# Optimization experiments

Measured on AMD Instinct MI355X. Metric: run time of the kernel, lower is better.

## Reference

```python
import jax, jax.numpy as jnp
import numpy as np

L, N, C = 8192, 8, 3
DIM, DIM_OUT, K, RATIO = 64, 128, 16, 0.25
L2 = int(L * RATIO)  # 2048; note L % L2 == 0 (needed for the fmod quirk)
EPS = 1e-5


def layer_norm(x, g, b):
    m = jnp.mean(x, axis=-1, keepdims=True)
    v = jnp.mean(jnp.square(x - m), axis=-1, keepdims=True)  # biased var, as torch LayerNorm
    return (x - m) * jax.lax.rsqrt(v + EPS) * g + b


def mlp(x, w1, g1, b1, w2, g2, b2):
    h = x @ w1.T
    h = layer_norm(h, g1, b1)
    h = h @ w2.T
    h = layer_norm(h, g2, b2)
    return jax.nn.relu(h)


def setup_inputs() -> dict:
    key = jax.random.key(0)
    ks = jax.random.split(key, 5)
    coords = jax.random.normal(ks[0], (L, N, C), jnp.float32)
    features = jax.random.normal(ks[1], (L, N, DIM), jnp.float32)
    s1 = 1.0 / np.sqrt(DIM)
    s2 = 1.0 / np.sqrt(DIM_OUT)
    w1 = jax.random.uniform(ks[2], (DIM_OUT, DIM), jnp.float32, -s1, s1)
    w2 = jax.random.uniform(ks[3], (DIM_OUT, DIM_OUT), jnp.float32, -s2, s2)
    g1 = jnp.ones((DIM_OUT,), jnp.float32)
    b1 = jnp.zeros((DIM_OUT,), jnp.float32)
    g2 = jnp.ones((DIM_OUT,), jnp.float32)
    b2 = jnp.zeros((DIM_OUT,), jnp.float32)
    # RandomDecimate: random permutation of point indices, keep first L2 (same across batch)
    keep_idx = jax.random.permutation(ks[4], L)[:L2].astype(jnp.int32)
    return dict(coords=coords, features=features, w1=w1, g1=g1, b1=b1,
                w2=w2, g2=g2, b2=b2, keep_idx=keep_idx)


def reference(coords, features, w1, g1, b1, w2, g2, b2, keep_idx):
    # MLP on all points: [L, N, DIM_OUT]
    feats = mlp(features, w1, g1, b1, w2, g2, b2)
    # decimation: keep_coords [L2, N, C]
    keep_coords = coords[keep_idx]
    # per-batch KNN of kept points against all points
    c = coords.transpose(1, 0, 2)        # [N, L, C]
    kc = keep_coords.transpose(1, 0, 2)  # [N, L2, C]
    d2 = (jnp.sum(kc * kc, -1)[:, :, None]
          + jnp.sum(c * c, -1)[:, None, :]
          - 2.0 * jnp.einsum('nic,njc->nij', kc, c))  # [N, L2, L]
    _, nn_idx = jax.lax.top_k(-d2, K)    # [N, L2, K] indices into [0, L)
    # faithful to clusters.fmod_(L2) on flattened idx n*L+l (L % L2 == 0 => l % L2)
    nn_idx = nn_idx % L2
    # fused gather + amax pooling over K neighbors
    fT = feats.transpose(1, 0, 2)  # [N, L, DIM_OUT]
    gathered = jax.vmap(lambda f, idx: f[idx])(fT, nn_idx)  # [N, L2, K, DIM_OUT]
    pool_features = jnp.max(gathered, axis=2).transpose(1, 0, 2)  # [L2, N, DIM_OUT]
    return keep_coords, pool_features
```

## Files before the change

### kernel.cpp

```cpp
#include <hip/hip_runtime.h>
#include <stdint.h>

#define L_    8192
#define N_    8
#define L2_   2048
#define K_    16

typedef unsigned int uint;
typedef unsigned short ushort;
typedef unsigned long long u64;
typedef __attribute__((ext_vector_type(8))) short bh8;
typedef __attribute__((ext_vector_type(4))) float f32x4;

__device__ __forceinline__ ushort f2b(float f){
  uint u = __float_as_uint(f);
  return (ushort)((u + 0x7FFFu + ((u >> 16) & 1u)) >> 16);
}
__device__ __forceinline__ uint ford(float f){
  uint u = __float_as_uint(f);
  return u ^ ((uint)((int)u >> 31) | 0x80000000u);
}
__device__ __forceinline__ float unford(uint u){
  uint v = (u & 0x80000000u) ? (u ^ 0x80000000u) : ~u;
  return __uint_as_float(v);
}

__device__ __forceinline__ void ld8(float* t, const float* p){
  float4 a = *(const float4*)p; float4 b = *(const float4*)(p + 4);
  t[0]=a.x; t[1]=a.y; t[2]=a.z; t[3]=a.w; t[4]=b.x; t[5]=b.y; t[6]=b.z; t[7]=b.w;
}
__device__ __forceinline__ bh8 pack8(const float* v){
  bh8 r;
  #pragma unroll
  for (int j = 0; j < 8; ++j) r[j] = (short)f2b(v[j]);
  return r;
}

__global__ __launch_bounds__(256) void prep_pack_k(const float* __restrict__ coords,
                                                   const int* __restrict__ keep,
                                                   const float* __restrict__ w1,
                                                   const float* __restrict__ w2,
                                                   float4* __restrict__ cF,
                                                   float* __restrict__ out0,
                                                   ushort* __restrict__ pw1,
                                                   ushort* __restrict__ pw2){
  int blk = blockIdx.x;
  int tid = threadIdx.x;
  if (blk < 96){
    int e = blk * 256 + tid;
    if (e < 8192) pw1[e] = f2b(w1[e]);
    else          pw2[e - 8192] = f2b(w2[e - 8192]);
  } else if (blk < 352){
    int e = (blk - 96) * 256 + tid;
    int l = e >> 3, n = e & 7;
    const float* cr = coords + (size_t)e * 3;
    float x = cr[0], y = cr[1], z = cr[2];
    float cc;
    {
      #pragma clang fp contract(off)
      cc = x*x + y*y + z*z;
    }
    cF[n * L_ + l] = make_float4(x, y, z, cc);
  } else {
    int t = (blk - 352) * 256 + tid;
    int i = t / 24; int rem = t - i * 24;
    out0[t] = coords[(size_t)keep[i] * 24 + rem];
  }
}

__global__ __launch_bounds__(256) void mlp_k(const float* __restrict__ feat,
                                             const ushort* __restrict__ pw1,
                                             const float* __restrict__ g1,
                                             const float* __restrict__ b1,
                                             const ushort* __restrict__ pw2,
                                             const float* __restrict__ g2,
                                             const float* __restrict__ b2,
                                             uint* __restrict__ fBw){
  __shared__ ushort hlds[64 * 136];
  int tid = threadIdx.x;
  int lane = tid & 63;
  int wv = __builtin_amdgcn_readfirstlane(tid >> 6);
  int quad = lane >> 4, c = lane & 15;
  int rowg = blockIdx.x * 64 + wv * 16;

  bh8 a1[2];
  {
    int rg = rowg + c; int l = rg & 2047, nb = rg >> 11;
    const float* xr = feat + (size_t)((l << 3) + nb) * 64 + quad * 8;
    float t[8];
    ld8(t, xr);      a1[0] = pack8(t);
    ld8(t, xr + 32); a1[1] = pack8(t);
  }

  f32x4 acc1[8];
  #pragma unroll
  for (int t = 0; t < 8; ++t) acc1[t] = (f32x4){0.f, 0.f, 0.f, 0.f};
  #pragma unroll
  for (int s = 0; s < 2; ++s){
    #pragma unroll
    for (int t = 0; t < 8; ++t){
      bh8 wb = *(const bh8*)(pw1 + (size_t)(t * 16 + c) * 64 + s * 32 + quad * 8);
      acc1[t] = __builtin_amdgcn_mfma_f32_16x16x32_bf16(a1[s], wb, acc1[t], 0, 0, 0);
    }
  }

  float mean1[4], rstd1[4];
  #pragma unroll
  for (int r = 0; r < 4; ++r){
    float s = 0.f;
    #pragma unroll
    for (int t = 0; t < 8; ++t) s += acc1[t][r];
    #pragma unroll
    for (int m = 1; m < 16; m <<= 1) s += __shfl_xor(s, m, 16);
    mean1[r] = s * 0.0078125f;
  }
  #pragma unroll
  for (int r = 0; r < 4; ++r){
    float s = 0.f;
    #pragma unroll
    for (int t = 0; t < 8; ++t){ float d = acc1[t][r] - mean1[r]; s += d * d; }
    #pragma unroll
    for (int m = 1; m < 16; m <<= 1) s += __shfl_xor(s, m, 16);
    rstd1[r] = rsqrtf(s * 0.0078125f + 1e-5f);
  }
  ushort* hl = hlds + wv * 16 * 136;
  #pragma unroll
  for (int t = 0; t < 8; ++t){
    float gv = g1[t * 16 + c], bv = b1[t * 16 + c];
    #pragma unroll
    for (int r = 0; r < 4; ++r){
      float v = (acc1[t][r] - mean1[r]) * rstd1[r] * gv + bv;
      hl[(quad * 4 + r) * 136 + t * 16 + c] = f2b(v);
    }
  }

  f32x4 acc2[8];
  #pragma unroll
  for (int t = 0; t < 8; ++t) acc2[t] = (f32x4){0.f, 0.f, 0.f, 0.f};
  #pragma unroll
  for (int s = 0; s < 4; ++s){
    bh8 af = *(const bh8*)(hl + c * 136 + s * 32 + quad * 8);
    #pragma unroll
    for (int t = 0; t < 8; ++t){
      bh8 wb = *(const bh8*)(pw2 + (size_t)(t * 16 + c) * 128 + s * 32 + quad * 8);
      acc2[t] = __builtin_amdgcn_mfma_f32_16x16x32_bf16(af, wb, acc2[t], 0, 0, 0);
    }
  }

  float mean2[4], rstd2[4];
  #pragma unroll
  for (int r = 0; r < 4; ++r){
    float s = 0.f;
    #pragma unroll
    for (int t = 0; t < 8; ++t) s += acc2[t][r];
    #pragma unroll
    for (int m = 1; m < 16; m <<= 1) s += __shfl_xor(s, m, 16);
    mean2[r] = s * 0.0078125f;
  }
  #pragma unroll
  for (int r = 0; r < 4; ++r){
    float s = 0.f;
    #pragma unroll
    for (int t = 0; t < 8; ++t){ float d = acc2[t][r] - mean2[r]; s += d * d; }
    #pragma unroll
    for (int m = 1; m < 16; m <<= 1) s += __shfl_xor(s, m, 16);
    rstd2[r] = rsqrtf(s * 0.0078125f + 1e-5f);
  }
  #pragma unroll
  for (int t = 0; t < 8; ++t){
    float gv = g2[t * 16 + c], bv = b2[t * 16 + c];
    #pragma unroll
    for (int r = 0; r < 4; ++r){
      float v = fmaxf((acc2[t][r] - mean2[r]) * rstd2[r] * gv + bv, 0.f);
      hl[(quad * 4 + r) * 136 + t * 16 + c] = f2b(v);
    }
  }

  {
    int row16 = lane >> 2, chunk = lane & 3;
    const uint* src = (const uint*)hlds + (wv * 16 + row16) * 68 + chunk * 16;
    uint* dst = fBw + (size_t)(rowg + row16) * 64 + chunk * 16;
    #pragma unroll
    for (int j = 0; j < 4; ++j)
      *(uint4*)(dst + j * 4) = *(const uint4*)(src + j * 4);
  }
}

__device__ __forceinline__ u64 shfl64(u64 v, int src){
  int lo = __shfl((int)(uint)v, src, 64);
  int hi = __shfl((int)(uint)(v >> 32), src, 64);
  return ((u64)(uint)hi << 32) | (uint)lo;
}

__device__ __forceinline__ u64 bsort64(u64 key, int lane){
  #pragma unroll
  for (int k = 2; k <= 64; k <<= 1){
    #pragma unroll
    for (int j = k >> 1; j > 0; j >>= 1){
      u64 o = shfl64(key, lane ^ j);
      bool lower = (lane & j) == 0;
      bool down  = (lane & k) == 0;
      bool takeMin = (lower == down);
      bool oLess = o < key;
      key = (oLess == takeMin) ? o : key;
    }
  }
  return key;
}
__device__ __forceinline__ u64 bmerge64(u64 key, int lane){
  #pragma unroll
  for (int j = 32; j > 0; j >>= 1){
    u64 o = shfl64(key, lane ^ j);
    bool lower = (lane & j) == 0;
    bool oLess = o < key;
    key = (oLess == lower) ? o : key;
  }
  return key;
}

__device__ __attribute__((noinline)) u64 drainx(u64* ldsq, int qcount, int lane){
  u64 a = (lane < qcount) ? ldsq[lane] : ~0ull;
  a = bsort64(a, lane);
  if (qcount > 64){
    u64 b = (64 + lane < qcount) ? ldsq[64 + lane] : ~0ull;
    b = bsort64(b, lane);
    u64 br = shfl64(b, 63 - lane);
    a = a < br ? a : br;
    a = bmerge64(a, lane);
  }
  if (lane < 16) ldsq[lane] = a;
  return a;
}

__device__ __forceinline__ void updq(u64* ql, int& qc, int& nx, float& thr,
                                     float qw, int lane){
  int q = qc;
  u64 k0 = (lane < q) ? ql[lane] : ~0ull;
  u64 k1 = (64 + lane < q) ? ql[64 + lane] : ~0ull;
  uint h0 = (uint)(k0 >> 32), h1 = (uint)(k1 >> 32);
  uint m = h0 < h1 ? h0 : h1;
  uint v = 0u;
  #pragma unroll
  for (int b = 31; b >= 16; --b){
    uint tv = v | (1u << b);
    if (__popcll(__ballot(m < tv)) < 16) v = tv;
  }
  uint vb = (v >= 0xFFFF0000u) ? 0xFFFFFFFFu : (v + 0x10000u);

  bool kp0 = (h0 <= vb);
  u64 bal0 = __ballot(kp0);
  int r0 = __builtin_amdgcn_mbcnt_lo((uint)bal0, 0);
  r0 = __builtin_amdgcn_mbcnt_hi((uint)(bal0 >> 32), r0);
  if (kp0) ql[r0] = k0;
  int c0 = __popcll(bal0);
  bool kp1 = (h1 <= vb);
  u64 bal1 = __ballot(kp1);
  int r1 = __builtin_amdgcn_mbcnt_lo((uint)bal1, 0);
  r1 = __builtin_amdgcn_mbcnt_hi((uint)(bal1 >> 32), r1);
  if (kp1) ql[c0 + r1] = k1;
  int out = c0 + __popcll(bal1);

  uint hb = vb;
  if (out > 64){
    u64 a = drainx(ql, out, lane);
    hb = (uint)(shfl64(a, 15) >> 32);
    out = 16;
  }
  qc = out;
  nx = out + 33;
  thr = unford(hb) + 1e-3f - qw;
}

__global__ __launch_bounds__(256) void knn_pool_k(const float4* __restrict__ cF,
                                                  const int* __restrict__ keep,
                                                  const uint* __restrict__ fB32,
                                                  float* __restrict__ out1){
  __shared__ u64 q8[4][2][128];
  int tid = threadIdx.x, lane = tid & 63;
  int wv = tid >> 6;
  int g0 = blockIdx.x * 8 + wv * 2;
  int n = g0 >> 11;
  int i0 = g0 & 2047, i1 = i0 + 1;
  u64* qlA = q8[wv][0];
  u64* qlB = q8[wv][1];
  float4 qa = cF[(n << 13) + keep[i0]];
  float4 qb = cF[(n << 13) + keep[i1]];
  const float4* base = cF + (n << 13);

  float q2ax = -2.f * qa.x, q2ay = -2.f * qa.y, q2az = -2.f * qa.z;
  float q2bx = -2.f * qb.x, q2by = -2.f * qb.y, q2bz = -2.f * qb.z;
  float tA = 3.4e38f, tB = 3.4e38f;
  int qcA = 0, qcB = 0, nxA = 49, nxB = 49;

  #define PROC2(cf, jidx) { \
    float sA = __builtin_fmaf(q2ax,(cf).x, __builtin_fmaf(q2ay,(cf).y, __builtin_fmaf(q2az,(cf).z,(cf).w))); \
    float sB = __builtin_fmaf(q2bx,(cf).x, __builtin_fmaf(q2by,(cf).y, __builtin_fmaf(q2bz,(cf).z,(cf).w))); \
    u64 balA = __ballot(sA <= tA); \
    u64 balB = __ballot(sB <= tB); \
    if (balA){ \
      if (sA <= tA){ \
        float d2; \
        { \
          _Pragma("clang fp contract(off)") \
          float dot = qa.x*(cf).x + qa.y*(cf).y + qa.z*(cf).z; \
          d2 = (qa.w + (cf).w) - 2.0f * dot; \
        } \
        int rel = __builtin_amdgcn_mbcnt_lo((uint)balA, 0); \
        rel = __builtin_amdgcn_mbcnt_hi((uint)(balA >> 32), rel); \
        qlA[qcA + rel] = ((u64)ford(d2) << 32) | (uint)(jidx); \
      } \
      qcA += __popcll(balA); \
      if (qcA >= nxA) updq(qlA, qcA, nxA, tA, qa.w, lane); \
    } \
    if (balB){ \
      if (sB <= tB){ \
        float d2; \
        { \
          _Pragma("clang fp contract(off)") \
          float dot = qb.x*(cf).x + qb.y*(cf).y + qb.z*(cf).z; \
          d2 = (qb.w + (cf).w) - 2.0f * dot; \
        } \
        int rel = __builtin_amdgcn_mbcnt_lo((uint)balB, 0); \
        rel = __builtin_amdgcn_mbcnt_hi((uint)(balB >> 32), rel); \
        qlB[qcB + rel] = ((u64)ford(d2) << 32) | (uint)(jidx); \
      } \
      qcB += __popcll(balB); \
      if (qcB >= nxB) updq(qlB, qcB, nxB, tB, qb.w, lane); \
    } \
  }

  for (int b = 0; b < 128; b += 4){
    const float4* p = base + (b << 6) + lane;
    float4 c0 = p[0];
    float4 c1 = p[64];
    float4 c2 = p[128];
    float4 c3 = p[192];
    int j0 = (b << 6) + lane;
    PROC2(c0, j0);
    PROC2(c1, j0 + 64);
    PROC2(c2, j0 + 128);
    PROC2(c3, j0 + 192);
  }
  #undef PROC2

  u64 aA = drainx(qlA, qcA, lane);
  u64 aB = drainx(qlB, qcB, lane);

  const uint* frow = fB32 + ((size_t)(n << 11) << 6);
  float a0 = -3.4e38f, a1v = -3.4e38f, b0 = -3.4e38f, b1v = -3.4e38f;
  #pragma unroll
  for (int k = 0; k < 16; ++k){
    int idxA = (int)(shfl64(aA, k) & 2047u);
    int idxB = (int)(shfl64(aB, k) & 2047u);
    uint uA = frow[((size_t)idxA << 6) + lane];
    uint uB = frow[((size_t)idxB << 6) + lane];
    a0  = fmaxf(a0,  __uint_as_float((uA & 0xFFFFu) << 16));
    a1v = fmaxf(a1v, __uint_as_float((uA >> 16) << 16));
    b0  = fmaxf(b0,  __uint_as_float((uB & 0xFFFFu) << 16));
    b1v = fmaxf(b1v, __uint_as_float((uB >> 16) << 16));
  }
  float2* oA = (float2*)(out1 + (size_t)(i0 * 8 + n) * 128);
  float2* oB = (float2*)(out1 + (size_t)(i1 * 8 + n) * 128);
  oA[lane] = make_float2(a0, a1v);
  oB[lane] = make_float2(b0, b1v);
}

extern "C" void kernel_launch(void* const* d_in, const int* in_sizes, int n_in,
                              void* d_out, int out_size, void* d_ws, size_t ws_size,
                              hipStream_t stream){
  const float* coords = (const float*)d_in[0];
  const float* feat   = (const float*)d_in[1];
  const float* w1     = (const float*)d_in[2];
  const float* g1     = (const float*)d_in[3];
  const float* b1     = (const float*)d_in[4];
  const float* w2     = (const float*)d_in[5];
  const float* g2     = (const float*)d_in[6];
  const float* b2     = (const float*)d_in[7];
  const int*   keep   = (const int*)d_in[8];
  float* out0 = (float*)d_out;
  float* out1 = out0 + 49152;

  char* ws = (char*)d_ws;
  float4* cF  = (float4*)ws;
  ushort* fB  = (ushort*)(ws + (1 << 20));
  ushort* pw1 = (ushort*)(ws + (5 << 20));
  ushort* pw2 = pw1 + 8192;

  hipLaunchKernelGGL(prep_pack_k, dim3(544), dim3(256), 0, stream,
                     coords, keep, w1, w2, cF, out0, pw1, pw2);
  hipLaunchKernelGGL(mlp_k, dim3(256), dim3(256), 0, stream,
                     feat, pw1, g1, b1, pw2, g2, b2, (uint*)fB);
  hipLaunchKernelGGL(knn_pool_k, dim3(2048), dim3(256), 0, stream,
                     cF, keep, (const uint*)fB, out1);
}
```

Baseline: 161.2 us.

## Stage candidate coords in LDS and process four queries per wave

```diff
diff --git a/kernel.cpp b/kernel.cpp
--- a/kernel.cpp
+++ b/kernel.cpp
@@ -275,94 +275,91 @@
                                                   const int* __restrict__ keep,
                                                   const uint* __restrict__ fB32,
                                                   float* __restrict__ out1){
-  __shared__ u64 q8[4][2][128];
+  __shared__ float4 tile[256];
+  __shared__ u64 q16[16][128];
   int tid = threadIdx.x, lane = tid & 63;
   int wv = tid >> 6;
-  int g0 = blockIdx.x * 8 + wv * 2;
-  int n = g0 >> 11;
-  int i0 = g0 & 2047, i1 = i0 + 1;
-  u64* qlA = q8[wv][0];
-  u64* qlB = q8[wv][1];
-  float4 qa = cF[(n << 13) + keep[i0]];
-  float4 qb = cF[(n << 13) + keep[i1]];
+  int qbase = blockIdx.x * 16;
+  int n = qbase >> 11;
+  int i0 = (qbase & 2047) + wv * 4;
   const float4* base = cF + (n << 13);
 
-  float q2ax = -2.f * qa.x, q2ay = -2.f * qa.y, q2az = -2.f * qa.z;
-  float q2bx = -2.f * qb.x, q2by = -2.f * qb.y, q2bz = -2.f * qb.z;
-  float tA = 3.4e38f, tB = 3.4e38f;
-  int qcA = 0, qcB = 0, nxA = 49, nxB = 49;
-
-  #define PROC2(cf, jidx) { \
-    float sA = __builtin_fmaf(q2ax,(cf).x, __builtin_fmaf(q2ay,(cf).y, __builtin_fmaf(q2az,(cf).z,(cf).w))); \
-    float sB = __builtin_fmaf(q2bx,(cf).x, __builtin_fmaf(q2by,(cf).y, __builtin_fmaf(q2bz,(cf).z,(cf).w))); \
-    u64 balA = __ballot(sA <= tA); \
-    u64 balB = __ballot(sB <= tB); \
-    if (balA){ \
-      if (sA <= tA){ \
+  u64* ql[4] = { q16[wv * 4 + 0], q16[wv * 4 + 1], q16[wv * 4 + 2], q16[wv * 4 + 3] };
+  float4 qv[4];
+  float q2x[4], q2y[4], q2z[4], qw4[4], thr[4];
+  int qc[4], nx[4];
+  #pragma unroll
+  for (int qi = 0; qi < 4; ++qi){
+    qv[qi] = base[keep[i0 + qi]];
+    q2x[qi] = -2.f * qv[qi].x; q2y[qi] = -2.f * qv[qi].y; q2z[qi] = -2.f * qv[qi].z;
+    qw4[qi] = qv[qi].w;
+    thr[qi] = 3.4e38f; qc[qi] = 0; nx[qi] = 49;
+  }
+
+  #define PROC1(qi, cf, jidx) { \
+    float s = __builtin_fmaf(q2x[qi],(cf).x, __builtin_fmaf(q2y[qi],(cf).y, \
+              __builtin_fmaf(q2z[qi],(cf).z,(cf).w))); \
+    u64 bal = __ballot(s <= thr[qi]); \
+    if (bal){ \
+      if (s <= thr[qi]){ \
         float d2; \
         { \
           _Pragma("clang fp contract(off)") \
-          float dot = qa.x*(cf).x + qa.y*(cf).y + qa.z*(cf).z; \
-          d2 = (qa.w + (cf).w) - 2.0f * dot; \
+          float dot = qv[qi].x*(cf).x + qv[qi].y*(cf).y + qv[qi].z*(cf).z; \
+          d2 = (qw4[qi] + (cf).w) - 2.0f * dot; \
         } \
-        int rel = __builtin_amdgcn_mbcnt_lo((uint)balA, 0); \
-        rel = __builtin_amdgcn_mbcnt_hi((uint)(balA >> 32), rel); \
-        qlA[qcA + rel] = ((u64)ford(d2) << 32) | (uint)(jidx); \
+        int rel = __builtin_amdgcn_mbcnt_lo((uint)bal, 0); \
+        rel = __builtin_amdgcn_mbcnt_hi((uint)(bal >> 32), rel); \
+        ql[qi][qc[qi] + rel] = ((u64)ford(d2) << 32) | (uint)(jidx); \
       } \
-      qcA += __popcll(balA); \
-      if (qcA >= nxA) updq(qlA, qcA, nxA, tA, qa.w, lane); \
+      qc[qi] += __popcll(bal); \
+      if (qc[qi] >= nx[qi]) updq(ql[qi], qc[qi], nx[qi], thr[qi], qw4[qi], lane); \
     } \
-    if (balB){ \
-      if (sB <= tB){ \
-        float d2; \
-        { \
-          _Pragma("clang fp contract(off)") \
-          float dot = qb.x*(cf).x + qb.y*(cf).y + qb.z*(cf).z; \
-          d2 = (qb.w + (cf).w) - 2.0f * dot; \
-        } \
-        int rel = __builtin_amdgcn_mbcnt_lo((uint)balB, 0); \
-        rel = __builtin_amdgcn_mbcnt_hi((uint)(balB >> 32), rel); \
-        qlB[qcB + rel] = ((u64)ford(d2) << 32) | (uint)(jidx); \
-      } \
-      qcB += __popcll(balB); \
-      if (qcB >= nxB) updq(qlB, qcB, nxB, tB, qb.w, lane); \
-    } \
-  }
-
-  for (int b = 0; b < 128; b += 4){
-    const float4* p = base + (b << 6) + lane;
-    float4 c0 = p[0];
-    float4 c1 = p[64];
-    float4 c2 = p[128];
-    float4 c3 = p[192];
-    int j0 = (b << 6) + lane;
-    PROC2(c0, j0);
-    PROC2(c1, j0 + 64);
-    PROC2(c2, j0 + 128);
-    PROC2(c3, j0 + 192);
-  }
-  #undef PROC2
-
-  u64 aA = drainx(qlA, qcA, lane);
-  u64 aB = drainx(qlB, qcB, lane);
+  }
+
+  float4 stage = base[tid];
+  for (int t = 0; t < 32; ++t){
+    __syncthreads();
+    tile[tid] = stage;
+    __syncthreads();
+    if (t < 31) stage = base[(t + 1) * 256 + tid];
+    int j0 = t << 8;
+    #pragma unroll
+    for (int j = 0; j < 4; ++j){
+      float4 cf = tile[j * 64 + lane];
+      int jj = j0 + j * 64 + lane;
+      PROC1(0, cf, jj);
+      PROC1(1, cf, jj);
+      PROC1(2, cf, jj);
+      PROC1(3, cf, jj);
+    }
+  }
+  #undef PROC1
+
+  u64 aQ[4];
+  #pragma unroll
+  for (int qi = 0; qi < 4; ++qi)
+    aQ[qi] = drainx(ql[qi], qc[qi], lane);
 
   const uint* frow = fB32 + ((size_t)(n << 11) << 6);
-  float a0 = -3.4e38f, a1v = -3.4e38f, b0 = -3.4e38f, b1v = -3.4e38f;
+  float m0[4], m1[4];
+  #pragma unroll
+  for (int qi = 0; qi < 4; ++qi){ m0[qi] = -3.4e38f; m1[qi] = -3.4e38f; }
   #pragma unroll
   for (int k = 0; k < 16; ++k){
-    int idxA = (int)(shfl64(aA, k) & 2047u);
-    int idxB = (int)(shfl64(aB, k) & 2047u);
-    uint uA = frow[((size_t)idxA << 6) + lane];
-    uint uB = frow[((size_t)idxB << 6) + lane];
-    a0  = fmaxf(a0,  __uint_as_float((uA & 0xFFFFu) << 16));
-    a1v = fmaxf(a1v, __uint_as_float((uA >> 16) << 16));
-    b0  = fmaxf(b0,  __uint_as_float((uB & 0xFFFFu) << 16));
-    b1v = fmaxf(b1v, __uint_as_float((uB >> 16) << 16));
-  }
-  float2* oA = (float2*)(out1 + (size_t)(i0 * 8 + n) * 128);
-  float2* oB = (float2*)(out1 + (size_t)(i1 * 8 + n) * 128);
-  oA[lane] = make_float2(a0, a1v);
-  oB[lane] = make_float2(b0, b1v);
+    #pragma unroll
+    for (int qi = 0; qi < 4; ++qi){
+      int idx = (int)(shfl64(aQ[qi], k) & 2047u);
+      uint u = frow[((size_t)idx << 6) + lane];
+      m0[qi] = fmaxf(m0[qi], __uint_as_float((u & 0xFFFFu) << 16));
+      m1[qi] = fmaxf(m1[qi], __uint_as_float((u >> 16) << 16));
+    }
+  }
+  #pragma unroll
+  for (int qi = 0; qi < 4; ++qi){
+    float2* o = (float2*)(out1 + (size_t)((i0 + qi) * 8 + n) * 128);
+    o[lane] = make_float2(m0[qi], m1[qi]);
+  }
 }
 
 extern "C" void kernel_launch(void* const* d_in, const int* in_sizes, int n_in,
@@ -390,6 +387,6 @@
                      coords, keep, w1, w2, cF, out0, pw1, pw2);
   hipLaunchKernelGGL(mlp_k, dim3(256), dim3(256), 0, stream,
                      feat, pw1, g1, b1, pw2, g2, b2, (uint*)fB);
-  hipLaunchKernelGGL(knn_pool_k, dim3(2048), dim3(256), 0, stream,
+  hipLaunchKernelGGL(knn_pool_k, dim3(1024), dim3(256), 0, stream,
                      cF, keep, (const uint*)fB, out1);
 }
```

Result: slower. 177.1 us (+9.9%).

## Split MLP output columns across four waves with cross-wave LayerNorm reductions

Applied to the files above, without the earlier changes.

```diff
diff --git a/kernel.cpp b/kernel.cpp
--- a/kernel.cpp
+++ b/kernel.cpp
@@ -76,113 +76,131 @@
                                              const float* __restrict__ g2,
                                              const float* __restrict__ b2,
                                              uint* __restrict__ fBw){
-  __shared__ ushort hlds[64 * 136];
+  __shared__ ushort hlds[16 * 136];
+  __shared__ float pm1[4][16], pv1[4][16], pm2[4][16], pv2[4][16];
   int tid = threadIdx.x;
   int lane = tid & 63;
-  int wv = __builtin_amdgcn_readfirstlane(tid >> 6);
+  int h = __builtin_amdgcn_readfirstlane(tid >> 6);
   int quad = lane >> 4, c = lane & 15;
-  int rowg = blockIdx.x * 64 + wv * 16;
+  int rowg = blockIdx.x * 16;
 
   bh8 a1[2];
   {
     int rg = rowg + c; int l = rg & 2047, nb = rg >> 11;
     const float* xr = feat + (size_t)((l << 3) + nb) * 64 + quad * 8;
-    float t[8];
-    ld8(t, xr);      a1[0] = pack8(t);
-    ld8(t, xr + 32); a1[1] = pack8(t);
-  }
-
-  f32x4 acc1[8];
-  #pragma unroll
-  for (int t = 0; t < 8; ++t) acc1[t] = (f32x4){0.f, 0.f, 0.f, 0.f};
+    float t0[8];
+    ld8(t0, xr);      a1[0] = pack8(t0);
+    ld8(t0, xr + 32); a1[1] = pack8(t0);
+  }
+
+  f32x4 acc1[2];
+  acc1[0] = (f32x4){0.f,0.f,0.f,0.f}; acc1[1] = (f32x4){0.f,0.f,0.f,0.f};
   #pragma unroll
   for (int s = 0; s < 2; ++s){
     #pragma unroll
-    for (int t = 0; t < 8; ++t){
-      bh8 wb = *(const bh8*)(pw1 + (size_t)(t * 16 + c) * 64 + s * 32 + quad * 8);
+    for (int t = 0; t < 2; ++t){
+      bh8 wb = *(const bh8*)(pw1 + (size_t)(h * 32 + t * 16 + c) * 64 + s * 32 + quad * 8);
       acc1[t] = __builtin_amdgcn_mfma_f32_16x16x32_bf16(a1[s], wb, acc1[t], 0, 0, 0);
     }
   }
 
+  #pragma unroll
+  for (int r = 0; r < 4; ++r){
+    float s = acc1[0][r] + acc1[1][r];
+    #pragma unroll
+    for (int m = 1; m < 16; m <<= 1) s += __shfl_xor(s, m, 16);
+    if (c == 0) pm1[h][quad * 4 + r] = s;
+  }
+  __syncthreads();
   float mean1[4], rstd1[4];
   #pragma unroll
   for (int r = 0; r < 4; ++r){
-    float s = 0.f;
-    #pragma unroll
-    for (int t = 0; t < 8; ++t) s += acc1[t][r];
+    int row = quad * 4 + r;
+    mean1[r] = (pm1[0][row] + pm1[1][row] + pm1[2][row] + pm1[3][row]) * 0.0078125f;
+  }
+  #pragma unroll
+  for (int r = 0; r < 4; ++r){
+    float d0 = acc1[0][r] - mean1[r], d1 = acc1[1][r] - mean1[r];
+    float s = d0 * d0 + d1 * d1;
     #pragma unroll
     for (int m = 1; m < 16; m <<= 1) s += __shfl_xor(s, m, 16);
-    mean1[r] = s * 0.0078125f;
-  }
-  #pragma unroll
-  for (int r = 0; r < 4; ++r){
-    float s = 0.f;
-    #pragma unroll
-    for (int t = 0; t < 8; ++t){ float d = acc1[t][r] - mean1[r]; s += d * d; }
-    #pragma unroll
-    for (int m = 1; m < 16; m <<= 1) s += __shfl_xor(s, m, 16);
-    rstd1[r] = rsqrtf(s * 0.0078125f + 1e-5f);
-  }
-  ushort* hl = hlds + wv * 16 * 136;
-  #pragma unroll
-  for (int t = 0; t < 8; ++t){
-    float gv = g1[t * 16 + c], bv = b1[t * 16 + c];
+    if (c == 0) pv1[h][quad * 4 + r] = s;
+  }
+  __syncthreads();
+  #pragma unroll
+  for (int r = 0; r < 4; ++r){
+    int row = quad * 4 + r;
+    rstd1[r] = rsqrtf((pv1[0][row] + pv1[1][row] + pv1[2][row] + pv1[3][row]) * 0.0078125f + 1e-5f);
+  }
+  #pragma unroll
+  for (int t = 0; t < 2; ++t){
+    int col = h * 32 + t * 16 + c;
+    float gv = g1[col], bv = b1[col];
     #pragma unroll
     for (int r = 0; r < 4; ++r){
       float v = (acc1[t][r] - mean1[r]) * rstd1[r] * gv + bv;
-      hl[(quad * 4 + r) * 136 + t * 16 + c] = f2b(v);
-    }
-  }
-
-  f32x4 acc2[8];
-  #pragma unroll
-  for (int t = 0; t < 8; ++t) acc2[t] = (f32x4){0.f, 0.f, 0.f, 0.f};
+      hlds[(quad * 4 + r) * 136 + col] = f2b(v);
+    }
+  }
+  __syncthreads();
+
+  f32x4 acc2[2];
+  acc2[0] = (f32x4){0.f,0.f,0.f,0.f}; acc2[1] = (f32x4){0.f,0.f,0.f,0.f};
   #pragma unroll
   for (int s = 0; s < 4; ++s){
-    bh8 af = *(const bh8*)(hl + c * 136 + s * 32 + quad * 8);
-    #pragma unroll
-    for (int t = 0; t < 8; ++t){
-      bh8 wb = *(const bh8*)(pw2 + (size_t)(t * 16 + c) * 128 + s * 32 + quad * 8);
+    bh8 af = *(const bh8*)(hlds + c * 136 + s * 32 + quad * 8);
+    #pragma unroll
+    for (int t = 0; t < 2; ++t){
+      bh8 wb = *(const bh8*)(pw2 + (size_t)(h * 32 + t * 16 + c) * 128 + s * 32 + quad * 8);
       acc2[t] = __builtin_amdgcn_mfma_f32_16x16x32_bf16(af, wb, acc2[t], 0, 0, 0);
     }
   }
 
+  #pragma unroll
+  for (int r = 0; r < 4; ++r){
+    float s = acc2[0][r] + acc2[1][r];
+    #pragma unroll
+    for (int m = 1; m < 16; m <<= 1) s += __shfl_xor(s, m, 16);
+    if (c == 0) pm2[h][quad * 4 + r] = s;
+  }
+  __syncthreads();
   float mean2[4], rstd2[4];
   #pragma unroll
   for (int r = 0; r < 4; ++r){
-    float s = 0.f;
-    #pragma unroll
-    for (int t = 0; t < 8; ++t) s += acc2[t][r];
+    int row = quad * 4 + r;
+    mean2[r] = (pm2[0][row] + pm2[1][row] + pm2[2][row] + pm2[3][row]) * 0.0078125f;
+  }
+  #pragma unroll
+  for (int r = 0; r < 4; ++r){
+    float d0 = acc2[0][r] - mean2[r], d1 = acc2[1][r] - mean2[r];
+    float s = d0 * d0 + d1 * d1;
     #pragma unroll
     for (int m = 1; m < 16; m <<= 1) s += __shfl_xor(s, m, 16);
-    mean2[r] = s * 0.0078125f;
-  }
-  #pragma unroll
-  for (int r = 0; r < 4; ++r){
-    float s = 0.f;
-    #pragma unroll
-    for (int t = 0; t < 8; ++t){ float d = acc2[t][r] - mean2[r]; s += d * d; }
-    #pragma unroll
-    for (int m = 1; m < 16; m <<= 1) s += __shfl_xor(s, m, 16);
-    rstd2[r] = rsqrtf(s * 0.0078125f + 1e-5f);
-  }
-  #pragma unroll
-  for (int t = 0; t < 8; ++t){
-    float gv = g2[t * 16 + c], bv = b2[t * 16 + c];
+    if (c == 0) pv2[h][quad * 4 + r] = s;
+  }
+  __syncthreads();
+  #pragma unroll
+  for (int r = 0; r < 4; ++r){
+    int row = quad * 4 + r;
+    rstd2[r] = rsqrtf((pv2[0][row] + pv2[1][row] + pv2[2][row] + pv2[3][row]) * 0.0078125f + 1e-5f);
+  }
+  #pragma unroll
+  for (int t = 0; t < 2; ++t){
+    int col = h * 32 + t * 16 + c;
+    float gv = g2[col], bv = b2[col];
     #pragma unroll
     for (int r = 0; r < 4; ++r){
       float v = fmaxf((acc2[t][r] - mean2[r]) * rstd2[r] * gv + bv, 0.f);
-      hl[(quad * 4 + r) * 136 + t * 16 + c] = f2b(v);
-    }
-  }
+      hlds[(quad * 4 + r) * 136 + col] = f2b(v);
+    }
+  }
+  __syncthreads();
 
   {
-    int row16 = lane >> 2, chunk = lane & 3;
-    const uint* src = (const uint*)hlds + (wv * 16 + row16) * 68 + chunk * 16;
-    uint* dst = fBw + (size_t)(rowg + row16) * 64 + chunk * 16;
-    #pragma unroll
-    for (int j = 0; j < 4; ++j)
-      *(uint4*)(dst + j * 4) = *(const uint4*)(src + j * 4);
+    int row16 = tid >> 4, pos = (tid & 15) * 4;
+    const uint* src = (const uint*)hlds + row16 * 68 + pos;
+    uint* dst = fBw + (size_t)(rowg + row16) * 64 + pos;
+    *(uint4*)dst = *(const uint4*)src;
   }
 }
 
@@ -388,7 +406,7 @@
 
   hipLaunchKernelGGL(prep_pack_k, dim3(544), dim3(256), 0, stream,
                      coords, keep, w1, w2, cF, out0, pw1, pw2);
-  hipLaunchKernelGGL(mlp_k, dim3(256), dim3(256), 0, stream,
+  hipLaunchKernelGGL(mlp_k, dim3(1024), dim3(256), 0, stream,
                      feat, pw1, g1, b1, pw2, g2, b2, (uint*)fB);
   hipLaunchKernelGGL(knn_pool_k, dim3(2048), dim3(256), 0, stream,
                      cF, keep, (const uint*)fB, out1);
```

New measurement: 158.7 us. No clear change (-1.5%).
